# Performance work log

Measured on AMD Instinct MI355X. Metric: run time of the kernel, lower is better.

The kernel has to match this reference:

```python
import jax, jax.numpy as jnp
import numpy as np

RADIX = 23                 # hidden_radix fixed-point fractional bits
SCALE = float(1 << RADIX)
F = 10                     # fractional bits used to quantize forget gates
FS = 1 << F
MAX_FORGET = 0.875
H = 512
D = H // 2
SLICE = 100
VOCAB = 32000
T, B = 512, 64
L = 2


def setup_inputs() -> dict:
    key = jax.random.key(0)
    ks = jax.random.split(key, 8)
    s = 0.06  # ~1/sqrt(768) init scale, keeps gates unsaturated
    return {
        "input_seq": jax.random.randint(ks[0], (T, B), 0, VOCAB),
        "lengths": jax.random.randint(ks[1], (B,), 1, T + 1),
        "emb": jax.random.normal(ks[2], (VOCAB, H), jnp.float32) * s,
        "Wz1": jax.random.normal(ks[3], (L, H + D, H), jnp.float32) * s,
        "bz1": jnp.zeros((L, H), jnp.float32),
        "Wg1": jax.random.normal(ks[4], (L, H + D, D), jnp.float32) * s,
        "bg1": jnp.zeros((L, D), jnp.float32),
        "Wz2": jax.random.normal(ks[5], (L, H + D, H), jnp.float32) * s,
        "bz2": jnp.zeros((L, H), jnp.float32),
        "Wg2": jax.random.normal(ks[6], (L, H + D, D), jnp.float32) * s,
        "bg2": jnp.zeros((L, D), jnp.float32),
    }


def _to_float(h_int):
    # ConvertToFloat: dequantize int fixed-point hidden (radix 23)
    return h_int.astype(jnp.float32) / SCALE


def _quant_gate(z):
    # restrict forgetting: z in [1 - max_forget, 1], then quantize to F frac bits
    z = MAX_FORGET * z + (1.0 - MAX_FORGET)
    return jnp.clip(jnp.floor(z * FS), 1, FS).astype(jnp.int32)


def _fixed_mul(h, zq):
    # exact floor(h * zq / 2**F) in int32 (no overflow): split h into hi/lo
    h_hi = h >> F               # arithmetic shift == floor division
    h_lo = h & (FS - 1)
    return h_hi * zq + ((h_lo * zq) >> F)


def _revgru_cell(x, h, Wz1, bz1, Wg1, bg1, Wz2, bz2, Wg2, bg2):
    # h: int32 [B, H] fixed-point hidden, split into reversible halves
    h1, h2 = h[:, :D], h[:, D:]
    h2f = _to_float(h2)
    zr1 = jax.nn.sigmoid(jnp.concatenate([x, h2f], 1) @ Wz1 + bz1)   # [B, H]
    zq1, r1 = _quant_gate(zr1[:, :D]), zr1[:, D:]
    z1f = zq1.astype(jnp.float32) / FS
    g1 = jnp.tanh(jnp.concatenate([x, r1 * h2f], 1) @ Wg1 + bg1)     # [B, D]
    h1 = _fixed_mul(h1, zq1) + jnp.round((1.0 - z1f) * g1 * SCALE).astype(jnp.int32)
    h1f = _to_float(h1)
    zr2 = jax.nn.sigmoid(jnp.concatenate([x, h1f], 1) @ Wz2 + bz2)
    zq2, r2 = _quant_gate(zr2[:, :D]), zr2[:, D:]
    z2f = zq2.astype(jnp.float32) / FS
    g2 = jnp.tanh(jnp.concatenate([x, r2 * h1f], 1) @ Wg2 + bg2)
    h2 = _fixed_mul(h2, zq2) + jnp.round((1.0 - z2f) * g2 * SCALE).astype(jnp.int32)
    return jnp.concatenate([h1, h2], 1)


def reference(input_seq, lengths, emb, Wz1, bz1, Wg1, bg1, Wz2, bz2, Wg2, bg2):
    input_seq = input_seq.astype(jnp.int32)
    xs = emb[input_seq]                                       # [T, B, H] (lockdropi p=0)
    mask = jnp.arange(T)[:, None] < lengths[None, :]          # [T, B]
    h0 = jnp.zeros((B, H), jnp.int32)
    cur = xs
    last_hiddens = []
    all_hs = None
    # stacked RNN: run each layer fully over time (equivalent to the t,l double loop)
    for l in range(L):
        def step(h, inp, l=l):
            x, m = inp
            hn = _revgru_cell(x, h, Wz1[l], bz1[l], Wg1[l], bg1[l],
                              Wz2[l], bz2[l], Wg2[l], bg2[l])
            hn = jnp.where(m[:, None], hn, h)                 # length masking
            return hn, hn
        hT, hs = jax.lax.scan(step, h0, (cur, mask))
        last_hiddens.append(hT)
        if l < L - 1:
            cur = _to_float(hs)                               # output_hidden (lockdroph p=0)
        else:
            all_hs = hs
    # saved_hiddens: top-layer hidden slice before each step plus final -> T+1 entries
    saved = jnp.concatenate([h0[None], all_hs], 0)[:, :, :SLICE]
    return jnp.stack(last_hiddens), saved
```

## Files before the change

kernel.cpp:

```cpp
#include <hip/hip_runtime.h>
#include <stdint.h>


typedef __attribute__((ext_vector_type(8))) short short8;
typedef __attribute__((ext_vector_type(4))) float floatx4;

#define MFMA16(a,b,c) __builtin_amdgcn_mfma_f32_16x16x32_bf16((a),(b),(c),0,0,0)

__device__ __forceinline__ short bf16_rne(float f) {
  uint32_t u = __float_as_uint(f);
  u += 0x7FFFu + ((u >> 16) & 1u);
  return (short)(u >> 16);
}
__device__ __forceinline__ float bf16f(short s) {
  return __uint_as_float(((uint32_t)(uint16_t)s) << 16);
}
__device__ __forceinline__ void st64(unsigned long long* p, unsigned long long v) {
  __hip_atomic_store(p, v, __ATOMIC_RELAXED, __HIP_MEMORY_SCOPE_AGENT);
}
__device__ __forceinline__ unsigned long long ld64(const unsigned long long* p) {
  return __hip_atomic_load(p, __ATOMIC_RELAXED, __HIP_MEMORY_SCOPE_AGENT);
}

#define SCALE_F 8388608.0f
#define INV_S   (1.0f/8388608.0f)

__device__ float g_X[50331648];
__device__ short g_WTh[2][786432];
__device__ short g_WTl[2][786432];
__device__ float g_biasL[2][1536];
__device__ unsigned long long g_ch[2][4][6][4096];
__device__ unsigned long long g_h0s[16777216];
__device__ unsigned long long g_x1r[3145728];
__device__ unsigned long long g_sent[2][4][4][8];
__device__ unsigned g_epoch;

__global__ void bump_epoch() { g_epoch = g_epoch + 1u; }

__global__ void prep_x(const float* __restrict__ Wz1, const float* __restrict__ bz1,
                       const float* __restrict__ Wg1, const float* __restrict__ bg1,
                       const float* __restrict__ Wz2, const float* __restrict__ bz2,
                       const float* __restrict__ Wg2, const float* __restrict__ bg2,
                       int layer, int* __restrict__ d_out, int zero_extra) {
  int idx = blockIdx.x * 256 + threadIdx.x;
  int k = idx / 1536;
  int c = idx - k * 1536;
  const float* W; const float* bb; int cc; int ncols;
  if (c < 512)       { W = Wz1; bb = bz1; cc = c;        ncols = 512; }
  else if (c < 768)  { W = Wg1; bb = bg1; cc = c - 512;  ncols = 256; }
  else if (c < 1280) { W = Wz2; bb = bz2; cc = c - 768;  ncols = 512; }
  else               { W = Wg2; bb = bg2; cc = c - 1280; ncols = 256; }
  float wv = W[(size_t)layer * 768 * ncols + (size_t)k * ncols + cc];
  short hi = bf16_rne(wv);
  short lo = bf16_rne(wv - bf16f(hi));
  g_WTh[layer][(size_t)c * 512 + k] = hi;
  g_WTl[layer][(size_t)c * 512 + k] = lo;
  if (k == 0) g_biasL[layer][c] = bb[layer * ncols + cc];
  if (zero_extra && idx < 6400) d_out[65536 + idx] = 0;
}

__global__ __launch_bounds__(256)
void gemmx_kernel(const int* __restrict__ seq, const float* __restrict__ emb) {
  __shared__ float At[128][36];
  __shared__ short Bhi[128][40];
  __shared__ short Blo[128][40];
  __shared__ int toks[128];
  int tid = threadIdx.x;
  int r0 = blockIdx.x * 128;
  int c0 = blockIdx.y * 128;
  if (tid < 128) toks[tid] = seq[r0 + tid];
  int lane = tid & 63;
  int wid = tid >> 6;
  int wm = wid & 1, wn = wid >> 1;
  int lm = lane & 15, lq = lane >> 4;
  floatx4 zero4 = {0.f, 0.f, 0.f, 0.f};
  floatx4 acc[4][4];
#pragma unroll
  for (int a = 0; a < 4; ++a)
#pragma unroll
    for (int b = 0; b < 4; ++b) acc[a][b] = zero4;
  __syncthreads();
  int am = tid >> 1;
  int ah = (tid & 1) * 16;
  const float* arow = emb + (size_t)toks[am] * 512;
  const short* bh_base = g_WTh[0] + (size_t)(c0 + am) * 512;
  const short* bl_base = g_WTl[0] + (size_t)(c0 + am) * 512;
  for (int kb = 0; kb < 16; ++kb) {
    int k0 = kb * 32 + ah;
    float4 a0 = *(const float4*)(arow + k0);
    float4 a1 = *(const float4*)(arow + k0 + 4);
    float4 a2 = *(const float4*)(arow + k0 + 8);
    float4 a3 = *(const float4*)(arow + k0 + 12);
    short4 b0 = *(const short4*)(bh_base + k0);
    short4 b1 = *(const short4*)(bh_base + k0 + 4);
    short4 b2 = *(const short4*)(bh_base + k0 + 8);
    short4 b3 = *(const short4*)(bh_base + k0 + 12);
    short4 l0 = *(const short4*)(bl_base + k0);
    short4 l1 = *(const short4*)(bl_base + k0 + 4);
    short4 l2 = *(const short4*)(bl_base + k0 + 8);
    short4 l3 = *(const short4*)(bl_base + k0 + 12);
    __syncthreads();
    *(float4*)&At[am][ah]      = a0;
    *(float4*)&At[am][ah + 4]  = a1;
    *(float4*)&At[am][ah + 8]  = a2;
    *(float4*)&At[am][ah + 12] = a3;
    *(short4*)&Bhi[am][ah]      = b0;
    *(short4*)&Bhi[am][ah + 4]  = b1;
    *(short4*)&Bhi[am][ah + 8]  = b2;
    *(short4*)&Bhi[am][ah + 12] = b3;
    *(short4*)&Blo[am][ah]      = l0;
    *(short4*)&Blo[am][ah + 4]  = l1;
    *(short4*)&Blo[am][ah + 8]  = l2;
    *(short4*)&Blo[am][ah + 12] = l3;
    __syncthreads();
    short8 afh[4], afl[4];
#pragma unroll
    for (int mt = 0; mt < 4; ++mt) {
      const float* ap = &At[wm*64 + mt*16 + lm][lq*8];
#pragma unroll
      for (int j = 0; j < 8; ++j) {
        float v = ap[j];
        short hi = bf16_rne(v);
        afh[mt][j] = hi;
        afl[mt][j] = bf16_rne(v - bf16f(hi));
      }
    }
#pragma unroll
    for (int nt = 0; nt < 4; ++nt) {
      short8 bfh = *(short8*)&Bhi[wn*64 + nt*16 + lm][lq*8];
      short8 bfl = *(short8*)&Blo[wn*64 + nt*16 + lm][lq*8];
#pragma unroll
      for (int mt = 0; mt < 4; ++mt) {
        acc[mt][nt] = MFMA16(afh[mt], bfh, acc[mt][nt]);
        acc[mt][nt] = MFMA16(afl[mt], bfh, acc[mt][nt]);
        acc[mt][nt] = MFMA16(afh[mt], bfl, acc[mt][nt]);
      }
    }
  }
#pragma unroll
  for (int nt = 0; nt < 4; ++nt) {
    int gc = c0 + wn*64 + nt*16 + lm;
    float bv = g_biasL[0][gc];
#pragma unroll
    for (int mt = 0; mt < 4; ++mt) {
#pragma unroll
      for (int i = 0; i < 4; ++i) {
        int gr = r0 + wm*64 + mt*16 + lq*4 + i;
        g_X[(size_t)gr * 1536 + gc] = acc[mt][nt][i] + bv;
      }
    }
  }
}

__global__ __launch_bounds__(512, 1)
void fused_kernel(const float* __restrict__ Wz1g, const float* __restrict__ Wg1g,
                  const float* __restrict__ Wz2g, const float* __restrict__ Wg2g,
                  const int* __restrict__ lengths, int* __restrict__ d_out) {
  __shared__ int   h1i[16][260];
  __shared__ int   h2i[16][260];
  __shared__ short phi[16][264];
  __shared__ short pmi[16][264];
  __shared__ short plo[16][264];
  __shared__ float redbuf[2304];
  __shared__ int lens[16];
  __shared__ short ahs[16][520];
  __shared__ short als[16][520];

  int tid = threadIdx.x;
  int bid = blockIdx.x;
  int lane = tid & 63, wv = tid >> 6;
  int lm = lane & 15, lq = lane >> 4;
  unsigned ep = g_epoch;

  if (bid >= 64) {
    int xw = bid - 64;
    int r4 = xw & 3;
    int cs = xw >> 2;
    int colx = cs * 128 + wv * 16 + lm;
    short8 bh[16], bl[16];
#pragma unroll
    for (int kf = 0; kf < 16; ++kf) {
      bh[kf] = *(const short8*)&g_WTh[1][(size_t)colx * 512 + kf * 32 + lq * 8];
      bl[kf] = *(const short8*)&g_WTl[1][(size_t)colx * 512 + kf * 32 + lq * 8];
    }
    float bvx = g_biasL[1][colx];

    for (int t = 0; t < 512; ++t) {
      unsigned tagt = (ep << 10) | (unsigned)(t + 1);
      if (tid < 8) {
        const unsigned long long* sp = &g_sent[0][r4][3][tid];
        while ((int)((unsigned)(ld64(sp) >> 32) - tagt) < 0) __builtin_amdgcn_s_sleep(1);
      }
      __syncthreads();
      {
        const unsigned long long* hp = &g_h0s[((size_t)t * 512 + tid) * 64 + r4 * 16];
        unsigned long long v[16];
        do { v[0] = ld64(hp); } while ((unsigned)(v[0] >> 32) != tagt);
#pragma unroll
        for (int i = 1; i < 16; ++i) v[i] = ld64(hp + i);
        unsigned pend = 0;
#pragma unroll
        for (int i = 1; i < 16; ++i)
          if ((unsigned)(v[i] >> 32) != tagt) pend |= 1u << i;
        while (pend) {
          __builtin_amdgcn_s_sleep(1);
#pragma unroll
          for (int i = 1; i < 16; ++i)
            if (pend & (1u << i)) {
              v[i] = ld64(hp + i);
              if ((unsigned)(v[i] >> 32) == tagt) pend &= ~(1u << i);
            }
        }
#pragma unroll
        for (int i = 0; i < 16; ++i) {
          float f = __uint_as_float((unsigned)v[i]);
          short hi = bf16_rne(f);
          ahs[i][tid] = hi;
          als[i][tid] = bf16_rne(f - bf16f(hi));
        }
      }
      __syncthreads();
      floatx4 acc = {0.f, 0.f, 0.f, 0.f};
#pragma unroll
      for (int kf = 0; kf < 16; ++kf) {
        short8 a0 = *(short8*)&ahs[lm][kf * 32 + lq * 8];
        short8 a1 = *(short8*)&als[lm][kf * 32 + lq * 8];
        acc = MFMA16(a0, bh[kf], acc);
        acc = MFMA16(a1, bh[kf], acc);
        acc = MFMA16(a0, bl[kf], acc);
      }
      if (t >= 25) {
        if (tid < 4) {
          unsigned need = (ep << 10) | (unsigned)(t - 24);
          while ((unsigned)(ld64(&g_ch[1][tid][5][0]) >> 32) < need) __builtin_amdgcn_s_sleep(2);
        }
      }
      __syncthreads();
#pragma unroll
      for (int i = 0; i < 4; ++i) {
        int row = r4 * 16 + lq * 4 + i;
        st64(&g_x1r[((size_t)(t & 31) * 64 + row) * 1536 + colx],
             ((unsigned long long)tagt << 32) | __float_as_uint(acc[i] + bvx));
      }
      __syncthreads();
    }
    return;
  }

  int grp = bid & 7;
  int cg  = bid >> 3;
  int L   = grp >> 2;
  int dm  = grp & 3;
  int rb0 = dm * 16;
  unsigned long long (*ch)[4096] = g_ch[L][dm];

  if (tid < 16) lens[tid] = lengths[rb0 + tid];
  for (int i = tid; i < 16 * 260; i += 512) { ((int*)h1i)[i] = 0; ((int*)h2i)[i] = 0; }

  short8 wz1a[4], wz1b[4], wz1c[4], wz2a[4], wz2b[4], wz2c[4];
  short8 wg1a[2], wg1b[2], wg2a[2], wg2b[2];
  {
    int nt = wv & 3, kh = wv >> 2;
    int colz = cg * 64 + nt * 16 + lm;
    const float* W1 = Wz1g + (size_t)L * 768 * 512 + (size_t)512 * 512 + colz;
    const float* W2 = Wz2g + (size_t)L * 768 * 512 + (size_t)512 * 512 + colz;
#pragma unroll
    for (int ks = 0; ks < 4; ++ks) {
      int k0 = kh * 128 + ks * 32 + lq * 8;
      short8 t0, t1, t2, u0, u1, u2;
#pragma unroll
      for (int j = 0; j < 8; ++j) {
        float v = W1[(size_t)(k0 + j) * 512] * INV_S;
        short a0 = bf16_rne(v); float r1 = v - bf16f(a0);
        short a1 = bf16_rne(r1); float r2 = r1 - bf16f(a1);
        t0[j] = a0; t1[j] = a1; t2[j] = bf16_rne(r2);
        float v2 = W2[(size_t)(k0 + j) * 512] * INV_S;
        short d0 = bf16_rne(v2); float s1 = v2 - bf16f(d0);
        short d1 = bf16_rne(s1); float s2 = s1 - bf16f(d1);
        u0[j] = d0; u1[j] = d1; u2[j] = bf16_rne(s2);
      }
      wz1a[ks] = t0; wz1b[ks] = t1; wz1c[ks] = t2;
      wz2a[ks] = u0; wz2b[ks] = u1; wz2c[ks] = u2;
    }
    int ntg = wv & 1, kq = wv >> 1;
    int colg = cg * 32 + ntg * 16 + lm;
    const float* G1 = Wg1g + (size_t)L * 768 * 256 + (size_t)512 * 256 + colg;
    const float* G2 = Wg2g + (size_t)L * 768 * 256 + (size_t)512 * 256 + colg;
#pragma unroll
    for (int ks = 0; ks < 2; ++ks) {
      int k0 = kq * 64 + ks * 32 + lq * 8;
      short8 t0, t1, u0, u1;
#pragma unroll
      for (int j = 0; j < 8; ++j) {
        float v = G1[(size_t)(k0 + j) * 256];
        short a0 = bf16_rne(v);
        t0[j] = a0; t1[j] = bf16_rne(v - bf16f(a0));
        float v2 = G2[(size_t)(k0 + j) * 256];
        short d0 = bf16_rne(v2);
        u0[j] = d0; u1[j] = bf16_rne(v2 - bf16f(d0));
      }
      wg1a[ks] = t0; wg1b[ks] = t1; wg2a[ks] = u0; wg2b[ks] = u1;
    }
  }
  __syncthreads();

  int xr = tid & 15, xc = tid >> 4;
  int scc = tid >> 1, sh = (tid & 1) << 3;

  int xo0 = cg * 64 + 2 * xc;
  int xo1 = 512 + cg * 32 + xc;
  int xo2 = 768 + cg * 64 + 2 * xc;
  int xo3 = 1280 + cg * 32 + xc;

  auto ldx = [&](int tt, float& za, float& zb, float& g1x, float& ya, float& yb, float& g2x) {
    const float* base = g_X + (size_t)(tt * 64 + rb0 + xr) * 1536;
    float2 v1 = *(const float2*)(base + cg * 64 + 2 * xc);
    za = v1.x; zb = v1.y;
    g1x = base[512 + cg * 32 + xc];
    float2 v2 = *(const float2*)(base + 768 + cg * 64 + 2 * xc);
    ya = v2.x; yb = v2.y;
    g2x = base[1280 + cg * 32 + xc];
  };
  float cz1a = 0.f, cz1b = 0.f, cg1x = 0.f, cz2a = 0.f, cz2b = 0.f, cg2x = 0.f;
  if (L == 0) ldx(0, cz1a, cz1b, cg1x, cz2a, cz2b, cg2x);

#define GATE(PH, NEED)                                                         \
  {                                                                            \
    if (tid < 8) {                                                             \
      const unsigned long long* sp_ = &g_sent[L][dm][PH][tid];                 \
      while ((int)((unsigned)(ld64(sp_) >> 32) - (NEED)) < 0)                  \
        __builtin_amdgcn_s_sleep(1);                                           \
    }                                                                          \
    __syncthreads();                                                           \
  }

#define STAGE8(CHIDX, EXP, DEPOSIT)                                            \
  {                                                                            \
    const unsigned long long* cp_ = &ch[CHIDX][scc * 16 + sh];                 \
    unsigned long long v_[8];                                                  \
    do { v_[0] = ld64(cp_); } while ((unsigned)(v_[0] >> 32) != (EXP));        \
    _Pragma("unroll")                                                          \
    for (int i_ = 1; i_ < 8; ++i_) v_[i_] = ld64(cp_ + i_);                    \
    unsigned pend_ = 0;                                                        \
    _Pragma("unroll")                                                          \
    for (int i_ = 1; i_ < 8; ++i_)                                             \
      if ((unsigned)(v_[i_] >> 32) != (EXP)) pend_ |= 1u << i_;                \
    while (pend_) {                                                            \
      __builtin_amdgcn_s_sleep(1);                                             \
      _Pragma("unroll")                                                        \
      for (int i_ = 1; i_ < 8; ++i_)                                           \
        if (pend_ & (1u << i_)) {                                              \
          v_[i_] = ld64(cp_ + i_);                                             \
          if ((unsigned)(v_[i_] >> 32) == (EXP)) pend_ &= ~(1u << i_);         \
        }                                                                      \
    }                                                                          \
    _Pragma("unroll")                                                          \
    for (int i_ = 0; i_ < 8; ++i_) { DEPOSIT; }                                \
  }

#define DEP_SPLIT(HARR)                                                        \
  { int hv_ = (int)(unsigned)v_[i_];                                           \
    HARR[sh + i_][scc] = hv_;                                                  \
    float fv_ = (float)hv_;                                                    \
    short a0_ = bf16_rne(fv_); float r1_ = fv_ - bf16f(a0_);                   \
    short a1_ = bf16_rne(r1_);                                                 \
    phi[sh + i_][scc] = a0_; pmi[sh + i_][scc] = a1_;                          \
    plo[sh + i_][scc] = bf16_rne(r1_ - bf16f(a1_)); }

#define DEP_R()                                                                \
  { unsigned pl_ = (unsigned)v_[i_];                                           \
    phi[sh + i_][scc] = (short)(pl_ >> 16);                                    \
    plo[sh + i_][scc] = (short)(pl_ & 0xFFFFu); }

#define SPLIT3Z(SRC)                                                           \
  {                                                                            \
    _Pragma("unroll")                                                          \
    for (int i_ = 0; i_ < 8; ++i_) {                                           \
      float v = (float)SRC[sh + i_][scc];                                      \
      short a0 = bf16_rne(v); float r1 = v - bf16f(a0);                        \
      short a1 = bf16_rne(r1);                                                 \
      phi[sh + i_][scc] = a0; pmi[sh + i_][scc] = a1;                          \
      plo[sh + i_][scc] = bf16_rne(r1 - bf16f(a1));                            \
    }                                                                          \
  }

  for (int t = 0; t < 512; ++t) {
    unsigned tagp = (ep << 10) | (unsigned)(t + 1);

    float nz1a, nz1b, ng1x, nz2a, nz2b, ng2x;
    if (L == 0) {
      int tn = (t + 1 < 512) ? t + 1 : t;
      ldx(tn, nz1a, nz1b, ng1x, nz2a, nz2b, ng2x);
    }

    const unsigned long long* xb = nullptr;
    unsigned long long x0v = 0, x1v = 0, x2v = 0, x3v = 0, x4v = 0, x5v = 0;
    if (L == 1) {
      xb = &g_x1r[((size_t)((t & 31) * 64) + rb0 + xr) * 1536];
      x0v = ld64(xb + xo0); x1v = ld64(xb + xo0 + 1);
      x2v = ld64(xb + xo1);
      x3v = ld64(xb + xo2); x4v = ld64(xb + xo2 + 1);
      x5v = ld64(xb + xo3);
    }
    auto vfy = [&](unsigned long long v, const unsigned long long* p) -> float {
      while ((unsigned)(v >> 32) != tagp) { __builtin_amdgcn_s_sleep(1); v = ld64(p); }
      return __uint_as_float((unsigned)v);
    };

    if (t > 0) {
      GATE(3, (ep << 10) | (unsigned)t);
      STAGE8(5, (ep << 10) | (unsigned)t, DEP_SPLIT(h2i));
    } else {
      SPLIT3Z(h2i);
    }
    __syncthreads();
    {
      int nt = wv & 3, kh = wv >> 2;
      floatx4 acc = {0.f, 0.f, 0.f, 0.f};
#pragma unroll
      for (int ks = 0; ks < 4; ++ks) {
        int k0 = kh * 128 + ks * 32 + lq * 8;
        short8 a0 = *(short8*)&phi[lm][k0];
        short8 a1 = *(short8*)&pmi[lm][k0];
        short8 a2 = *(short8*)&plo[lm][k0];
        acc = MFMA16(a0, wz1a[ks], acc);
        acc = MFMA16(a0, wz1b[ks], acc);
        acc = MFMA16(a1, wz1a[ks], acc);
        acc = MFMA16(a1, wz1b[ks], acc);
        acc = MFMA16(a0, wz1c[ks], acc);
        acc = MFMA16(a2, wz1a[ks], acc);
      }
#pragma unroll
      for (int i = 0; i < 4; ++i) redbuf[kh * 1088 + (lq * 4 + i) * 68 + nt * 16 + lm] = acc[i];
    }
    __syncthreads();
    {
      if (L == 1) { cz1a = vfy(x0v, xb + xo0); cz1b = vfy(x1v, xb + xo0 + 1); }
#pragma unroll
      for (int u = 0; u < 2; ++u) {
        int cc = 2 * xc + u;
        float pre = redbuf[xr * 68 + cc] + redbuf[1088 + xr * 68 + cc] + (u ? cz1b : cz1a);
        float s = 1.0f / (1.0f + expf(-pre));
        int gcol = cg * 64 + cc;
        if (gcol < 256) {
          float qf = floorf((0.875f * s + 0.125f) * 1024.0f);
          int qi = (int)qf; qi = qi < 1 ? 1 : (qi > 1024 ? 1024 : qi);
          st64(&ch[0][gcol * 16 + xr], ((unsigned long long)tagp << 32) | (unsigned)qi);
        } else {
          int rc = gcol - 256;
          float p = s * ((float)h2i[xr][rc] * INV_S);
          short p0 = bf16_rne(p);
          short p1s = bf16_rne(p - bf16f(p0));
          unsigned pay = ((unsigned)(unsigned short)p0 << 16) | (unsigned)(unsigned short)p1s;
          st64(&ch[1][rc * 16 + xr], ((unsigned long long)tagp << 32) | pay);
        }
      }
    }
    __syncthreads();
    if (tid == 0) st64(&g_sent[L][dm][0][cg], ((unsigned long long)tagp << 32) | 1u);
    GATE(0, tagp);

    int qv;
    STAGE8(1, tagp, DEP_R());
    {
      const unsigned long long* qp = &ch[0][(cg * 32 + xc) * 16 + xr];
      unsigned long long q64;
      do { q64 = ld64(qp); } while ((unsigned)(q64 >> 32) != tagp);
      qv = (int)(unsigned)q64;
    }
    __syncthreads();
    {
      int ntg = wv & 1, kq = wv >> 1;
      floatx4 acc = {0.f, 0.f, 0.f, 0.f};
#pragma unroll
      for (int ks = 0; ks < 2; ++ks) {
        int k0 = kq * 64 + ks * 32 + lq * 8;
        short8 a0 = *(short8*)&phi[lm][k0];
        short8 a1 = *(short8*)&plo[lm][k0];
        acc = MFMA16(a0, wg1a[ks], acc);
        acc = MFMA16(a1, wg1a[ks], acc);
        acc = MFMA16(a0, wg1b[ks], acc);
      }
#pragma unroll
      for (int i = 0; i < 4; ++i) redbuf[kq * 576 + (lq * 4 + i) * 36 + ntg * 16 + lm] = acc[i];
    }
    __syncthreads();
    {
      if (L == 1) cg1x = vfy(x2v, xb + xo1);
      float pre = redbuf[xr * 36 + xc] + redbuf[576 + xr * 36 + xc]
                + redbuf[1152 + xr * 36 + xc] + redbuf[1728 + xr * 36 + xc] + cg1x;
      float g = tanhf(pre);
      int gc = cg * 32 + xc;
      int q = qv;
      int hold = h1i[xr][gc];
      float zf = (float)q * (1.0f / 1024.0f);
      int ni = (int)rintf((1.0f - zf) * g * SCALE_F);
      int hnew = (hold >> 10) * q + (((hold & 1023) * q) >> 10) + ni;
      if (t >= lens[xr]) hnew = hold;
      st64(&ch[2][gc * 16 + xr], ((unsigned long long)tagp << 32) | (unsigned)hnew);
      if (L == 0)
        st64(&g_h0s[((size_t)t * 512 + gc) * 64 + rb0 + xr],
             ((unsigned long long)tagp << 32) | __float_as_uint((float)hnew * INV_S));
      else if (gc < 100) d_out[65536 + (t + 1) * 6400 + (rb0 + xr) * 100 + gc] = hnew;
      if (t == 511) d_out[L * 32768 + (rb0 + xr) * 512 + gc] = hnew;
    }
    __syncthreads();
    if (tid == 0) st64(&g_sent[L][dm][1][cg], ((unsigned long long)tagp << 32) | 1u);
    GATE(1, tagp);

    STAGE8(2, tagp, DEP_SPLIT(h1i));
    __syncthreads();
    {
      int nt = wv & 3, kh = wv >> 2;
      floatx4 acc = {0.f, 0.f, 0.f, 0.f};
#pragma unroll
      for (int ks = 0; ks < 4; ++ks) {
        int k0 = kh * 128 + ks * 32 + lq * 8;
        short8 a0 = *(short8*)&phi[lm][k0];
        short8 a1 = *(short8*)&pmi[lm][k0];
        short8 a2 = *(short8*)&plo[lm][k0];
        acc = MFMA16(a0, wz2a[ks], acc);
        acc = MFMA16(a0, wz2b[ks], acc);
        acc = MFMA16(a1, wz2a[ks], acc);
        acc = MFMA16(a1, wz2b[ks], acc);
        acc = MFMA16(a0, wz2c[ks], acc);
        acc = MFMA16(a2, wz2a[ks], acc);
      }
#pragma unroll
      for (int i = 0; i < 4; ++i) redbuf[kh * 1088 + (lq * 4 + i) * 68 + nt * 16 + lm] = acc[i];
    }
    __syncthreads();
    {
      if (L == 1) { cz2a = vfy(x3v, xb + xo2); cz2b = vfy(x4v, xb + xo2 + 1); }
#pragma unroll
      for (int u = 0; u < 2; ++u) {
        int cc = 2 * xc + u;
        float pre = redbuf[xr * 68 + cc] + redbuf[1088 + xr * 68 + cc] + (u ? cz2b : cz2a);
        float s = 1.0f / (1.0f + expf(-pre));
        int gcol = cg * 64 + cc;
        if (gcol < 256) {
          float qf = floorf((0.875f * s + 0.125f) * 1024.0f);
          int qi = (int)qf; qi = qi < 1 ? 1 : (qi > 1024 ? 1024 : qi);
          st64(&ch[3][gcol * 16 + xr], ((unsigned long long)tagp << 32) | (unsigned)qi);
        } else {
          int rc = gcol - 256;
          float p = s * ((float)h1i[xr][rc] * INV_S);
          short p0 = bf16_rne(p);
          short p1s = bf16_rne(p - bf16f(p0));
          unsigned pay = ((unsigned)(unsigned short)p0 << 16) | (unsigned)(unsigned short)p1s;
          st64(&ch[4][rc * 16 + xr], ((unsigned long long)tagp << 32) | pay);
        }
      }
    }
    __syncthreads();
    if (tid == 0) st64(&g_sent[L][dm][2][cg], ((unsigned long long)tagp << 32) | 1u);
    GATE(2, tagp);

    int qv2;
    STAGE8(4, tagp, DEP_R());
    {
      const unsigned long long* qp = &ch[3][(cg * 32 + xc) * 16 + xr];
      unsigned long long q64;
      do { q64 = ld64(qp); } while ((unsigned)(q64 >> 32) != tagp);
      qv2 = (int)(unsigned)q64;
    }
    __syncthreads();
    {
      int ntg = wv & 1, kq = wv >> 1;
      floatx4 acc = {0.f, 0.f, 0.f, 0.f};
#pragma unroll
      for (int ks = 0; ks < 2; ++ks) {
        int k0 = kq * 64 + ks * 32 + lq * 8;
        short8 a0 = *(short8*)&phi[lm][k0];
        short8 a1 = *(short8*)&plo[lm][k0];
        acc = MFMA16(a0, wg2a[ks], acc);
        acc = MFMA16(a1, wg2a[ks], acc);
        acc = MFMA16(a0, wg2b[ks], acc);
      }
#pragma unroll
      for (int i = 0; i < 4; ++i) redbuf[kq * 576 + (lq * 4 + i) * 36 + ntg * 16 + lm] = acc[i];
    }
    __syncthreads();
    {
      if (L == 1) cg2x = vfy(x5v, xb + xo3);
      float pre = redbuf[xr * 36 + xc] + redbuf[576 + xr * 36 + xc]
                + redbuf[1152 + xr * 36 + xc] + redbuf[1728 + xr * 36 + xc] + cg2x;
      float g = tanhf(pre);
      int gc = cg * 32 + xc;
      int q = qv2;
      int hold = h2i[xr][gc];
      float zf = (float)q * (1.0f / 1024.0f);
      int ni = (int)rintf((1.0f - zf) * g * SCALE_F);
      int hnew = (hold >> 10) * q + (((hold & 1023) * q) >> 10) + ni;
      if (t >= lens[xr]) hnew = hold;
      st64(&ch[5][gc * 16 + xr], ((unsigned long long)tagp << 32) | (unsigned)hnew);
      if (L == 0)
        st64(&g_h0s[((size_t)t * 512 + 256 + gc) * 64 + rb0 + xr],
             ((unsigned long long)tagp << 32) | __float_as_uint((float)hnew * INV_S));
      if (t == 511) d_out[L * 32768 + (rb0 + xr) * 512 + 256 + gc] = hnew;
    }
    __syncthreads();
    if (tid == 0) st64(&g_sent[L][dm][3][cg], ((unsigned long long)tagp << 32) | 1u);

    if (L == 0) {
      cz1a = nz1a; cz1b = nz1b; cg1x = ng1x; cz2a = nz2a; cz2b = nz2b; cg2x = ng2x;
    }
  }
#undef GATE
#undef STAGE8
#undef DEP_SPLIT
#undef DEP_R
#undef SPLIT3Z
}

extern "C" void kernel_launch(void* const* d_in, const int* in_sizes, int n_in,
                              void* d_out, int out_size, void* d_ws, size_t ws_size,
                              hipStream_t stream) {
  const int*   seq     = (const int*)d_in[0];
  const int*   lengths = (const int*)d_in[1];
  const float* emb     = (const float*)d_in[2];
  const float* Wz1     = (const float*)d_in[3];
  const float* bz1     = (const float*)d_in[4];
  const float* Wg1     = (const float*)d_in[5];
  const float* bg1     = (const float*)d_in[6];
  const float* Wz2     = (const float*)d_in[7];
  const float* bz2     = (const float*)d_in[8];
  const float* Wg2     = (const float*)d_in[9];
  const float* bg2     = (const float*)d_in[10];
  int* out = (int*)d_out;
  (void)in_sizes; (void)n_in; (void)out_size; (void)d_ws; (void)ws_size;

  bump_epoch<<<1, 1, 0, stream>>>();
  prep_x<<<3072, 256, 0, stream>>>(Wz1, bz1, Wg1, bg1, Wz2, bz2, Wg2, bg2, 0, out, 1);
  prep_x<<<3072, 256, 0, stream>>>(Wz1, bz1, Wg1, bg1, Wz2, bz2, Wg2, bg2, 1, out, 0);
  gemmx_kernel<<<dim3(256, 12), 256, 0, stream>>>(seq, emb);
  fused_kernel<<<112, 512, 0, stream>>>(Wz1, Wg1, Wz2, Wg2, lengths, out);
}
```

Before: 7.788 ms.

## Assign whole-K gate tiles per wave and signal per-wave flags instead of block barriers

```diff
diff --git a/kernel.cpp b/kernel.cpp
--- a/kernel.cpp
+++ b/kernel.cpp
@@ -4,8 +4,10 @@
 
 typedef __attribute__((ext_vector_type(8))) short short8;
 typedef __attribute__((ext_vector_type(4))) float floatx4;
+typedef unsigned long long ull;
 
 #define MFMA16(a,b,c) __builtin_amdgcn_mfma_f32_16x16x32_bf16((a),(b),(c),0,0,0)
+#define DRAIN() asm volatile("s_waitcnt vmcnt(0)" ::: "memory")
 
 __device__ __forceinline__ short bf16_rne(float f) {
   uint32_t u = __float_as_uint(f);
@@ -15,10 +17,10 @@
 __device__ __forceinline__ float bf16f(short s) {
   return __uint_as_float(((uint32_t)(uint16_t)s) << 16);
 }
-__device__ __forceinline__ void st64(unsigned long long* p, unsigned long long v) {
+__device__ __forceinline__ void st64(ull* p, ull v) {
   __hip_atomic_store(p, v, __ATOMIC_RELAXED, __HIP_MEMORY_SCOPE_AGENT);
 }
-__device__ __forceinline__ unsigned long long ld64(const unsigned long long* p) {
+__device__ __forceinline__ ull ld64(const ull* p) {
   return __hip_atomic_load(p, __ATOMIC_RELAXED, __HIP_MEMORY_SCOPE_AGENT);
 }
 
@@ -29,10 +31,10 @@
 __device__ short g_WTh[2][786432];
 __device__ short g_WTl[2][786432];
 __device__ float g_biasL[2][1536];
-__device__ unsigned long long g_ch[2][4][6][4096];
-__device__ unsigned long long g_h0s[16777216];
-__device__ unsigned long long g_x1r[3145728];
-__device__ unsigned long long g_sent[2][4][4][8];
+__device__ ull g_ch[2][4][6][4096];
+__device__ ull g_h0s[16777216];
+__device__ ull g_x1r[3145728];
+__device__ ull g_sw[2][4][4][8][4];
 __device__ unsigned g_epoch;
 
 __global__ void bump_epoch() { g_epoch = g_epoch + 1u; }
@@ -161,7 +163,6 @@
   __shared__ short phi[16][264];
   __shared__ short pmi[16][264];
   __shared__ short plo[16][264];
-  __shared__ float redbuf[2304];
   __shared__ int lens[16];
   __shared__ short ahs[16][520];
   __shared__ short als[16][520];
@@ -187,14 +188,14 @@
 
     for (int t = 0; t < 512; ++t) {
       unsigned tagt = (ep << 10) | (unsigned)(t + 1);
-      if (tid < 8) {
-        const unsigned long long* sp = &g_sent[0][r4][3][tid];
+      if (tid < 16) {
+        const ull* sp = &g_sw[0][r4][3][tid & 7][tid >> 3];
         while ((int)((unsigned)(ld64(sp) >> 32) - tagt) < 0) __builtin_amdgcn_s_sleep(1);
       }
       __syncthreads();
       {
-        const unsigned long long* hp = &g_h0s[((size_t)t * 512 + tid) * 64 + r4 * 16];
-        unsigned long long v[16];
+        const ull* hp = &g_h0s[((size_t)t * 512 + tid) * 64 + r4 * 16];
+        ull v[16];
         do { v[0] = ld64(hp); } while ((unsigned)(v[0] >> 32) != tagt);
 #pragma unroll
         for (int i = 1; i < 16; ++i) v[i] = ld64(hp + i);
@@ -240,7 +241,7 @@
       for (int i = 0; i < 4; ++i) {
         int row = r4 * 16 + lq * 4 + i;
         st64(&g_x1r[((size_t)(t & 31) * 64 + row) * 1536 + colx],
-             ((unsigned long long)tagt << 32) | __float_as_uint(acc[i] + bvx));
+             ((ull)tagt << 32) | __float_as_uint(acc[i] + bvx));
       }
       __syncthreads();
     }
@@ -252,82 +253,70 @@
   int L   = grp >> 2;
   int dm  = grp & 3;
   int rb0 = dm * 16;
-  unsigned long long (*ch)[4096] = g_ch[L][dm];
+  ull (*ch)[4096] = g_ch[L][dm];
+
+  bool gw = (wv == 0 || wv == 1 || wv == 4 || wv == 5);
+  int zt = wv & 3;
+  int zcol = cg * 64 + zt * 16 + lm;
+  int zxcol = (wv < 4 ? 0 : 768) + zcol;
+  int gcolh = cg * 32 + (wv & 1) * 16 + lm;
+  int gxcol = (wv < 4 ? 512 : 1280) + gcolh;
 
   if (tid < 16) lens[tid] = lengths[rb0 + tid];
   for (int i = tid; i < 16 * 260; i += 512) { ((int*)h1i)[i] = 0; ((int*)h2i)[i] = 0; }
 
-  short8 wz1a[4], wz1b[4], wz1c[4], wz2a[4], wz2b[4], wz2c[4];
-  short8 wg1a[2], wg1b[2], wg2a[2], wg2b[2];
+  short8 wgt[24], wgtg[16];
   {
-    int nt = wv & 3, kh = wv >> 2;
-    int colz = cg * 64 + nt * 16 + lm;
-    const float* W1 = Wz1g + (size_t)L * 768 * 512 + (size_t)512 * 512 + colz;
-    const float* W2 = Wz2g + (size_t)L * 768 * 512 + (size_t)512 * 512 + colz;
-#pragma unroll
-    for (int ks = 0; ks < 4; ++ks) {
-      int k0 = kh * 128 + ks * 32 + lq * 8;
-      short8 t0, t1, t2, u0, u1, u2;
+    const float* Wz = (wv < 4) ? Wz1g : Wz2g;
+    const float* Wp = Wz + (size_t)L * 768 * 512 + (size_t)512 * 512 + zcol;
+#pragma unroll
+    for (int ks = 0; ks < 8; ++ks) {
+      short8 t0, t1, t2;
 #pragma unroll
       for (int j = 0; j < 8; ++j) {
-        float v = W1[(size_t)(k0 + j) * 512] * INV_S;
+        float v = Wp[(size_t)(ks * 32 + lq * 8 + j) * 512] * INV_S;
         short a0 = bf16_rne(v); float r1 = v - bf16f(a0);
-        short a1 = bf16_rne(r1); float r2 = r1 - bf16f(a1);
-        t0[j] = a0; t1[j] = a1; t2[j] = bf16_rne(r2);
-        float v2 = W2[(size_t)(k0 + j) * 512] * INV_S;
-        short d0 = bf16_rne(v2); float s1 = v2 - bf16f(d0);
-        short d1 = bf16_rne(s1); float s2 = s1 - bf16f(d1);
-        u0[j] = d0; u1[j] = d1; u2[j] = bf16_rne(s2);
-      }
-      wz1a[ks] = t0; wz1b[ks] = t1; wz1c[ks] = t2;
-      wz2a[ks] = u0; wz2b[ks] = u1; wz2c[ks] = u2;
-    }
-    int ntg = wv & 1, kq = wv >> 1;
-    int colg = cg * 32 + ntg * 16 + lm;
-    const float* G1 = Wg1g + (size_t)L * 768 * 256 + (size_t)512 * 256 + colg;
-    const float* G2 = Wg2g + (size_t)L * 768 * 256 + (size_t)512 * 256 + colg;
-#pragma unroll
-    for (int ks = 0; ks < 2; ++ks) {
-      int k0 = kq * 64 + ks * 32 + lq * 8;
-      short8 t0, t1, u0, u1;
-#pragma unroll
-      for (int j = 0; j < 8; ++j) {
-        float v = G1[(size_t)(k0 + j) * 256];
-        short a0 = bf16_rne(v);
-        t0[j] = a0; t1[j] = bf16_rne(v - bf16f(a0));
-        float v2 = G2[(size_t)(k0 + j) * 256];
-        short d0 = bf16_rne(v2);
-        u0[j] = d0; u1[j] = bf16_rne(v2 - bf16f(d0));
-      }
-      wg1a[ks] = t0; wg1b[ks] = t1; wg2a[ks] = u0; wg2b[ks] = u1;
+        short a1 = bf16_rne(r1);
+        t0[j] = a0; t1[j] = a1; t2[j] = bf16_rne(r1 - bf16f(a1));
+      }
+      wgt[ks * 3 + 0] = t0; wgt[ks * 3 + 1] = t1; wgt[ks * 3 + 2] = t2;
+    }
+    if (gw) {
+      const float* Wg = (wv < 4) ? Wg1g : Wg2g;
+      const float* Gp = Wg + (size_t)L * 768 * 256 + (size_t)512 * 256 + gcolh;
+#pragma unroll
+      for (int ks = 0; ks < 8; ++ks) {
+        short8 t0, t1;
+#pragma unroll
+        for (int j = 0; j < 8; ++j) {
+          float v = Gp[(size_t)(ks * 32 + lq * 8 + j) * 256];
+          short a0 = bf16_rne(v);
+          t0[j] = a0; t1[j] = bf16_rne(v - bf16f(a0));
+        }
+        wgtg[ks * 2 + 0] = t0; wgtg[ks * 2 + 1] = t1;
+      }
     }
   }
   __syncthreads();
 
-  int xr = tid & 15, xc = tid >> 4;
   int scc = tid >> 1, sh = (tid & 1) << 3;
 
-  int xo0 = cg * 64 + 2 * xc;
-  int xo1 = 512 + cg * 32 + xc;
-  int xo2 = 768 + cg * 64 + 2 * xc;
-  int xo3 = 1280 + cg * 32 + xc;
-
-  auto ldx = [&](int tt, float& za, float& zb, float& g1x, float& ya, float& yb, float& g2x) {
-    const float* base = g_X + (size_t)(tt * 64 + rb0 + xr) * 1536;
-    float2 v1 = *(const float2*)(base + cg * 64 + 2 * xc);
-    za = v1.x; zb = v1.y;
-    g1x = base[512 + cg * 32 + xc];
-    float2 v2 = *(const float2*)(base + 768 + cg * 64 + 2 * xc);
-    ya = v2.x; yb = v2.y;
-    g2x = base[1280 + cg * 32 + xc];
-  };
-  float cz1a = 0.f, cz1b = 0.f, cg1x = 0.f, cz2a = 0.f, cz2b = 0.f, cg2x = 0.f;
-  if (L == 0) ldx(0, cz1a, cz1b, cg1x, cz2a, cz2b, cg2x);
-
-#define GATE(PH, NEED)                                                         \
+  float xzc[4], xgc[4];
+  if (L == 0) {
+#pragma unroll
+    for (int i = 0; i < 4; ++i)
+      xzc[i] = g_X[(size_t)(rb0 + lq * 4 + i) * 1536 + zxcol];
+    if (gw) {
+#pragma unroll
+      for (int i = 0; i < 4; ++i)
+        xgc[i] = g_X[(size_t)(rb0 + lq * 4 + i) * 1536 + gxcol];
+    }
+  }
+
+#define GATEW(PH, NS, NEED)                                                    \
   {                                                                            \
-    if (tid < 8) {                                                             \
-      const unsigned long long* sp_ = &g_sent[L][dm][PH][tid];                 \
+    if (tid < 8 * (NS)) {                                                      \
+      const ull* sp_ = &g_sw[L][dm][PH][tid & 7][tid >> 3];                    \
       while ((int)((unsigned)(ld64(sp_) >> 32) - (NEED)) < 0)                  \
         __builtin_amdgcn_s_sleep(1);                                           \
     }                                                                          \
@@ -336,8 +325,8 @@
 
 #define STAGE8(CHIDX, EXP, DEPOSIT)                                            \
   {                                                                            \
-    const unsigned long long* cp_ = &ch[CHIDX][scc * 16 + sh];                 \
-    unsigned long long v_[8];                                                  \
+    const ull* cp_ = &ch[CHIDX][scc * 16 + sh];                                \
+    ull v_[8];                                                                 \
     do { v_[0] = ld64(cp_); } while ((unsigned)(v_[0] >> 32) != (EXP));        \
     _Pragma("unroll")                                                          \
     for (int i_ = 1; i_ < 8; ++i_) v_[i_] = ld64(cp_ + i_);                    \
@@ -387,226 +376,222 @@
   for (int t = 0; t < 512; ++t) {
     unsigned tagp = (ep << 10) | (unsigned)(t + 1);
 
-    float nz1a, nz1b, ng1x, nz2a, nz2b, ng2x;
+    float xzn[4], xgn[4];
     if (L == 0) {
       int tn = (t + 1 < 512) ? t + 1 : t;
-      ldx(tn, nz1a, nz1b, ng1x, nz2a, nz2b, ng2x);
-    }
-
-    const unsigned long long* xb = nullptr;
-    unsigned long long x0v = 0, x1v = 0, x2v = 0, x3v = 0, x4v = 0, x5v = 0;
+#pragma unroll
+      for (int i = 0; i < 4; ++i)
+        xzn[i] = g_X[(size_t)(tn * 64 + rb0 + lq * 4 + i) * 1536 + zxcol];
+      if (gw) {
+#pragma unroll
+        for (int i = 0; i < 4; ++i)
+          xgn[i] = g_X[(size_t)(tn * 64 + rb0 + lq * 4 + i) * 1536 + gxcol];
+      }
+    }
+
+    const ull* pzb = nullptr; const ull* pgb = nullptr;
+    ull xzv[4], xgv[4];
     if (L == 1) {
-      xb = &g_x1r[((size_t)((t & 31) * 64) + rb0 + xr) * 1536];
-      x0v = ld64(xb + xo0); x1v = ld64(xb + xo0 + 1);
-      x2v = ld64(xb + xo1);
-      x3v = ld64(xb + xo2); x4v = ld64(xb + xo2 + 1);
-      x5v = ld64(xb + xo3);
-    }
-    auto vfy = [&](unsigned long long v, const unsigned long long* p) -> float {
+      size_t rbase = (size_t)((t & 31) * 64) + rb0 + lq * 4;
+      pzb = &g_x1r[rbase * 1536 + zxcol];
+#pragma unroll
+      for (int i = 0; i < 4; ++i) xzv[i] = ld64(pzb + (size_t)i * 1536);
+      if (gw) {
+        pgb = &g_x1r[rbase * 1536 + gxcol];
+#pragma unroll
+        for (int i = 0; i < 4; ++i) xgv[i] = ld64(pgb + (size_t)i * 1536);
+      }
+    }
+    auto vfy = [&](ull v, const ull* p) -> float {
       while ((unsigned)(v >> 32) != tagp) { __builtin_amdgcn_s_sleep(1); v = ld64(p); }
       return __uint_as_float((unsigned)v);
     };
 
     if (t > 0) {
-      GATE(3, (ep << 10) | (unsigned)t);
+      GATEW(3, 2, (ep << 10) | (unsigned)t);
       STAGE8(5, (ep << 10) | (unsigned)t, DEP_SPLIT(h2i));
     } else {
       SPLIT3Z(h2i);
     }
     __syncthreads();
-    {
-      int nt = wv & 3, kh = wv >> 2;
+    if (wv < 4) {
       floatx4 acc = {0.f, 0.f, 0.f, 0.f};
 #pragma unroll
-      for (int ks = 0; ks < 4; ++ks) {
-        int k0 = kh * 128 + ks * 32 + lq * 8;
+      for (int ks = 0; ks < 8; ++ks) {
+        int k0 = ks * 32 + lq * 8;
         short8 a0 = *(short8*)&phi[lm][k0];
         short8 a1 = *(short8*)&pmi[lm][k0];
         short8 a2 = *(short8*)&plo[lm][k0];
-        acc = MFMA16(a0, wz1a[ks], acc);
-        acc = MFMA16(a0, wz1b[ks], acc);
-        acc = MFMA16(a1, wz1a[ks], acc);
-        acc = MFMA16(a1, wz1b[ks], acc);
-        acc = MFMA16(a0, wz1c[ks], acc);
-        acc = MFMA16(a2, wz1a[ks], acc);
-      }
-#pragma unroll
-      for (int i = 0; i < 4; ++i) redbuf[kh * 1088 + (lq * 4 + i) * 68 + nt * 16 + lm] = acc[i];
-    }
-    __syncthreads();
-    {
-      if (L == 1) { cz1a = vfy(x0v, xb + xo0); cz1b = vfy(x1v, xb + xo0 + 1); }
-#pragma unroll
-      for (int u = 0; u < 2; ++u) {
-        int cc = 2 * xc + u;
-        float pre = redbuf[xr * 68 + cc] + redbuf[1088 + xr * 68 + cc] + (u ? cz1b : cz1a);
-        float s = 1.0f / (1.0f + expf(-pre));
-        int gcol = cg * 64 + cc;
-        if (gcol < 256) {
+        acc = MFMA16(a0, wgt[ks*3+0], acc);
+        acc = MFMA16(a0, wgt[ks*3+1], acc);
+        acc = MFMA16(a1, wgt[ks*3+0], acc);
+        acc = MFMA16(a1, wgt[ks*3+1], acc);
+        acc = MFMA16(a0, wgt[ks*3+2], acc);
+        acc = MFMA16(a2, wgt[ks*3+0], acc);
+      }
+#pragma unroll
+      for (int i = 0; i < 4; ++i) {
+        int ri = lq * 4 + i;
+        float xv = (L == 0) ? xzc[i] : vfy(xzv[i], pzb + (size_t)i * 1536);
+        float s = 1.0f / (1.0f + expf(-(acc[i] + xv)));
+        if (zcol < 256) {
           float qf = floorf((0.875f * s + 0.125f) * 1024.0f);
           int qi = (int)qf; qi = qi < 1 ? 1 : (qi > 1024 ? 1024 : qi);
-          st64(&ch[0][gcol * 16 + xr], ((unsigned long long)tagp << 32) | (unsigned)qi);
+          st64(&ch[0][zcol * 16 + ri], ((ull)tagp << 32) | (unsigned)qi);
         } else {
-          int rc = gcol - 256;
-          float p = s * ((float)h2i[xr][rc] * INV_S);
+          int rc = zcol - 256;
+          float p = s * ((float)h2i[ri][rc] * INV_S);
           short p0 = bf16_rne(p);
           short p1s = bf16_rne(p - bf16f(p0));
           unsigned pay = ((unsigned)(unsigned short)p0 << 16) | (unsigned)(unsigned short)p1s;
-          st64(&ch[1][rc * 16 + xr], ((unsigned long long)tagp << 32) | pay);
-        }
-      }
-    }
+          st64(&ch[1][rc * 16 + ri], ((ull)tagp << 32) | pay);
+        }
+      }
+      DRAIN();
+      if (lane == 0) st64(&g_sw[L][dm][0][cg][zt], ((ull)tagp << 32) | 1u);
+    }
+
+    GATEW(0, 4, tagp);
+    STAGE8(1, tagp, DEP_R());
     __syncthreads();
-    if (tid == 0) st64(&g_sent[L][dm][0][cg], ((unsigned long long)tagp << 32) | 1u);
-    GATE(0, tagp);
-
-    int qv;
-    STAGE8(1, tagp, DEP_R());
-    {
-      const unsigned long long* qp = &ch[0][(cg * 32 + xc) * 16 + xr];
-      unsigned long long q64;
-      do { q64 = ld64(qp); } while ((unsigned)(q64 >> 32) != tagp);
-      qv = (int)(unsigned)q64;
-    }
-    __syncthreads();
-    {
-      int ntg = wv & 1, kq = wv >> 1;
+    if (wv < 2) {
       floatx4 acc = {0.f, 0.f, 0.f, 0.f};
 #pragma unroll
-      for (int ks = 0; ks < 2; ++ks) {
-        int k0 = kq * 64 + ks * 32 + lq * 8;
+      for (int ks = 0; ks < 8; ++ks) {
+        int k0 = ks * 32 + lq * 8;
         short8 a0 = *(short8*)&phi[lm][k0];
         short8 a1 = *(short8*)&plo[lm][k0];
-        acc = MFMA16(a0, wg1a[ks], acc);
-        acc = MFMA16(a1, wg1a[ks], acc);
-        acc = MFMA16(a0, wg1b[ks], acc);
-      }
-#pragma unroll
-      for (int i = 0; i < 4; ++i) redbuf[kq * 576 + (lq * 4 + i) * 36 + ntg * 16 + lm] = acc[i];
-    }
-    __syncthreads();
-    {
-      if (L == 1) cg1x = vfy(x2v, xb + xo1);
-      float pre = redbuf[xr * 36 + xc] + redbuf[576 + xr * 36 + xc]
-                + redbuf[1152 + xr * 36 + xc] + redbuf[1728 + xr * 36 + xc] + cg1x;
-      float g = tanhf(pre);
-      int gc = cg * 32 + xc;
-      int q = qv;
-      int hold = h1i[xr][gc];
-      float zf = (float)q * (1.0f / 1024.0f);
-      int ni = (int)rintf((1.0f - zf) * g * SCALE_F);
-      int hnew = (hold >> 10) * q + (((hold & 1023) * q) >> 10) + ni;
-      if (t >= lens[xr]) hnew = hold;
-      st64(&ch[2][gc * 16 + xr], ((unsigned long long)tagp << 32) | (unsigned)hnew);
-      if (L == 0)
-        st64(&g_h0s[((size_t)t * 512 + gc) * 64 + rb0 + xr],
-             ((unsigned long long)tagp << 32) | __float_as_uint((float)hnew * INV_S));
-      else if (gc < 100) d_out[65536 + (t + 1) * 6400 + (rb0 + xr) * 100 + gc] = hnew;
-      if (t == 511) d_out[L * 32768 + (rb0 + xr) * 512 + gc] = hnew;
-    }
-    __syncthreads();
-    if (tid == 0) st64(&g_sent[L][dm][1][cg], ((unsigned long long)tagp << 32) | 1u);
-    GATE(1, tagp);
-
+        acc = MFMA16(a0, wgtg[ks*2+0], acc);
+        acc = MFMA16(a1, wgtg[ks*2+0], acc);
+        acc = MFMA16(a0, wgtg[ks*2+1], acc);
+      }
+      const ull* qp = &ch[0][gcolh * 16 + lq * 4];
+      ull q64[4];
+#pragma unroll
+      for (int i = 0; i < 4; ++i) q64[i] = ld64(qp + i);
+#pragma unroll
+      for (int i = 0; i < 4; ++i)
+        while ((unsigned)(q64[i] >> 32) != tagp) {
+          __builtin_amdgcn_s_sleep(1); q64[i] = ld64(qp + i);
+        }
+#pragma unroll
+      for (int i = 0; i < 4; ++i) {
+        int ri = lq * 4 + i;
+        float xv = (L == 0) ? xgc[i] : vfy(xgv[i], pgb + (size_t)i * 1536);
+        float g = tanhf(acc[i] + xv);
+        int q = (int)(unsigned)q64[i];
+        int hold = h1i[ri][gcolh];
+        float zf = (float)q * (1.0f / 1024.0f);
+        int ni = (int)rintf((1.0f - zf) * g * SCALE_F);
+        int hnew = (hold >> 10) * q + (((hold & 1023) * q) >> 10) + ni;
+        if (t >= lens[ri]) hnew = hold;
+        h1i[ri][gcolh] = hnew;
+        st64(&ch[2][gcolh * 16 + ri], ((ull)tagp << 32) | (unsigned)hnew);
+        if (L == 0)
+          st64(&g_h0s[((size_t)t * 512 + gcolh) * 64 + rb0 + ri],
+               ((ull)tagp << 32) | __float_as_uint((float)hnew * INV_S));
+        else if (gcolh < 100) d_out[65536 + (t + 1) * 6400 + (rb0 + ri) * 100 + gcolh] = hnew;
+        if (t == 511) d_out[L * 32768 + (rb0 + ri) * 512 + gcolh] = hnew;
+      }
+      DRAIN();
+      if (lane == 0) st64(&g_sw[L][dm][1][cg][wv], ((ull)tagp << 32) | 1u);
+    }
+
+    GATEW(1, 2, tagp);
     STAGE8(2, tagp, DEP_SPLIT(h1i));
     __syncthreads();
-    {
-      int nt = wv & 3, kh = wv >> 2;
+    if (wv >= 4) {
       floatx4 acc = {0.f, 0.f, 0.f, 0.f};
 #pragma unroll
-      for (int ks = 0; ks < 4; ++ks) {
-        int k0 = kh * 128 + ks * 32 + lq * 8;
+      for (int ks = 0; ks < 8; ++ks) {
+        int k0 = ks * 32 + lq * 8;
         short8 a0 = *(short8*)&phi[lm][k0];
         short8 a1 = *(short8*)&pmi[lm][k0];
         short8 a2 = *(short8*)&plo[lm][k0];
-        acc = MFMA16(a0, wz2a[ks], acc);
-        acc = MFMA16(a0, wz2b[ks], acc);
-        acc = MFMA16(a1, wz2a[ks], acc);
-        acc = MFMA16(a1, wz2b[ks], acc);
-        acc = MFMA16(a0, wz2c[ks], acc);
-        acc = MFMA16(a2, wz2a[ks], acc);
-      }
-#pragma unroll
-      for (int i = 0; i < 4; ++i) redbuf[kh * 1088 + (lq * 4 + i) * 68 + nt * 16 + lm] = acc[i];
-    }
-    __syncthreads();
-    {
-      if (L == 1) { cz2a = vfy(x3v, xb + xo2); cz2b = vfy(x4v, xb + xo2 + 1); }
-#pragma unroll
-      for (int u = 0; u < 2; ++u) {
-        int cc = 2 * xc + u;
-        float pre = redbuf[xr * 68 + cc] + redbuf[1088 + xr * 68 + cc] + (u ? cz2b : cz2a);
-        float s = 1.0f / (1.0f + expf(-pre));
-        int gcol = cg * 64 + cc;
-        if (gcol < 256) {
+        acc = MFMA16(a0, wgt[ks*3+0], acc);
+        acc = MFMA16(a0, wgt[ks*3+1], acc);
+        acc = MFMA16(a1, wgt[ks*3+0], acc);
+        acc = MFMA16(a1, wgt[ks*3+1], acc);
+        acc = MFMA16(a0, wgt[ks*3+2], acc);
+        acc = MFMA16(a2, wgt[ks*3+0], acc);
+      }
+#pragma unroll
+      for (int i = 0; i < 4; ++i) {
+        int ri = lq * 4 + i;
+        float xv = (L == 0) ? xzc[i] : vfy(xzv[i], pzb + (size_t)i * 1536);
+        float s = 1.0f / (1.0f + expf(-(acc[i] + xv)));
+        if (zcol < 256) {
           float qf = floorf((0.875f * s + 0.125f) * 1024.0f);
           int qi = (int)qf; qi = qi < 1 ? 1 : (qi > 1024 ? 1024 : qi);
-          st64(&ch[3][gcol * 16 + xr], ((unsigned long long)tagp << 32) | (unsigned)qi);
+          st64(&ch[3][zcol * 16 + ri], ((ull)tagp << 32) | (unsigned)qi);
         } else {
-          int rc = gcol - 256;
-          float p = s * ((float)h1i[xr][rc] * INV_S);
+          int rc = zcol - 256;
+          float p = s * ((float)h1i[ri][rc] * INV_S);
           short p0 = bf16_rne(p);
           short p1s = bf16_rne(p - bf16f(p0));
           unsigned pay = ((unsigned)(unsigned short)p0 << 16) | (unsigned)(unsigned short)p1s;
-          st64(&ch[4][rc * 16 + xr], ((unsigned long long)tagp << 32) | pay);
-        }
-      }
-    }
+          st64(&ch[4][rc * 16 + ri], ((ull)tagp << 32) | pay);
+        }
+      }
+      DRAIN();
+      if (lane == 0) st64(&g_sw[L][dm][2][cg][zt], ((ull)tagp << 32) | 1u);
+    }
+
+    GATEW(2, 4, tagp);
+    STAGE8(4, tagp, DEP_R());
     __syncthreads();
-    if (tid == 0) st64(&g_sent[L][dm][2][cg], ((unsigned long long)tagp << 32) | 1u);
-    GATE(2, tagp);
-
-    int qv2;
-    STAGE8(4, tagp, DEP_R());
-    {
-      const unsigned long long* qp = &ch[3][(cg * 32 + xc) * 16 + xr];
-      unsigned long long q64;
-      do { q64 = ld64(qp); } while ((unsigned)(q64 >> 32) != tagp);
-      qv2 = (int)(unsigned)q64;
-    }
-    __syncthreads();
-    {
-      int ntg = wv & 1, kq = wv >> 1;
+    if (wv == 4 || wv == 5) {
       floatx4 acc = {0.f, 0.f, 0.f, 0.f};
 #pragma unroll
-      for (int ks = 0; ks < 2; ++ks) {
-        int k0 = kq * 64 + ks * 32 + lq * 8;
+      for (int ks = 0; ks < 8; ++ks) {
+        int k0 = ks * 32 + lq * 8;
         short8 a0 = *(short8*)&phi[lm][k0];
         short8 a1 = *(short8*)&plo[lm][k0];
-        acc = MFMA16(a0, wg2a[ks], acc);
-        acc = MFMA16(a1, wg2a[ks], acc);
-        acc = MFMA16(a0, wg2b[ks], acc);
-      }
-#pragma unroll
-      for (int i = 0; i < 4; ++i) redbuf[kq * 576 + (lq * 4 + i) * 36 + ntg * 16 + lm] = acc[i];
-    }
-    __syncthreads();
-    {
-      if (L == 1) cg2x = vfy(x5v, xb + xo3);
-      float pre = redbuf[xr * 36 + xc] + redbuf[576 + xr * 36 + xc]
-                + redbuf[1152 + xr * 36 + xc] + redbuf[1728 + xr * 36 + xc] + cg2x;
-      float g = tanhf(pre);
-      int gc = cg * 32 + xc;
-      int q = qv2;
-      int hold = h2i[xr][gc];
-      float zf = (float)q * (1.0f / 1024.0f);
-      int ni = (int)rintf((1.0f - zf) * g * SCALE_F);
-      int hnew = (hold >> 10) * q + (((hold & 1023) * q) >> 10) + ni;
-      if (t >= lens[xr]) hnew = hold;
-      st64(&ch[5][gc * 16 + xr], ((unsigned long long)tagp << 32) | (unsigned)hnew);
-      if (L == 0)
-        st64(&g_h0s[((size_t)t * 512 + 256 + gc) * 64 + rb0 + xr],
-             ((unsigned long long)tagp << 32) | __float_as_uint((float)hnew * INV_S));
-      if (t == 511) d_out[L * 32768 + (rb0 + xr) * 512 + 256 + gc] = hnew;
-    }
-    __syncthreads();
-    if (tid == 0) st64(&g_sent[L][dm][3][cg], ((unsigned long long)tagp << 32) | 1u);
+        acc = MFMA16(a0, wgtg[ks*2+0], acc);
+        acc = MFMA16(a1, wgtg[ks*2+0], acc);
+        acc = MFMA16(a0, wgtg[ks*2+1], acc);
+      }
+      const ull* qp = &ch[3][gcolh * 16 + lq * 4];
+      ull q64[4];
+#pragma unroll
+      for (int i = 0; i < 4; ++i) q64[i] = ld64(qp + i);
+#pragma unroll
+      for (int i = 0; i < 4; ++i)
+        while ((unsigned)(q64[i] >> 32) != tagp) {
+          __builtin_amdgcn_s_sleep(1); q64[i] = ld64(qp + i);
+        }
+#pragma unroll
+      for (int i = 0; i < 4; ++i) {
+        int ri = lq * 4 + i;
+        float xv = (L == 0) ? xgc[i] : vfy(xgv[i], pgb + (size_t)i * 1536);
+        float g = tanhf(acc[i] + xv);
+        int q = (int)(unsigned)q64[i];
+        int hold = h2i[ri][gcolh];
+        float zf = (float)q * (1.0f / 1024.0f);
+        int ni = (int)rintf((1.0f - zf) * g * SCALE_F);
+        int hnew = (hold >> 10) * q + (((hold & 1023) * q) >> 10) + ni;
+        if (t >= lens[ri]) hnew = hold;
+        h2i[ri][gcolh] = hnew;
+        st64(&ch[5][gcolh * 16 + ri], ((ull)tagp << 32) | (unsigned)hnew);
+        if (L == 0)
+          st64(&g_h0s[((size_t)t * 512 + 256 + gcolh) * 64 + rb0 + ri],
+               ((ull)tagp << 32) | __float_as_uint((float)hnew * INV_S));
+        if (t == 511) d_out[L * 32768 + (rb0 + ri) * 512 + 256 + gcolh] = hnew;
+      }
+      DRAIN();
+      if (lane == 0) st64(&g_sw[L][dm][3][cg][wv - 4], ((ull)tagp << 32) | 1u);
+    }
 
     if (L == 0) {
-      cz1a = nz1a; cz1b = nz1b; cg1x = ng1x; cz2a = nz2a; cz2b = nz2b; cg2x = ng2x;
-    }
-  }
-#undef GATE
+#pragma unroll
+      for (int i = 0; i < 4; ++i) { xzc[i] = xzn[i]; }
+      if (gw) {
+#pragma unroll
+        for (int i = 0; i < 4; ++i) { xgc[i] = xgn[i]; }
+      }
+    }
+  }
+#undef GATEW
 #undef STAGE8
 #undef DEP_SPLIT
 #undef DEP_R
```

Result: slower. 13.69 ms (+75.8%).
